# Kernel optimization log

Measured on AMD Instinct MI355X. Metric: run time of the kernel, lower is better.

The kernel has to match this reference:

```python
import jax, jax.numpy as jnp
import numpy as np

S = 4096
F = 512  # in_features, head_num == 1 so per-head dim == F


def setup_inputs() -> dict:
    key = jax.random.key(0)
    ks = jax.random.split(key, 11)
    std = 0.02
    inp = {
        "q": jax.random.normal(ks[0], (1, S, F), jnp.float32),
        "k": jax.random.normal(ks[1], (1, S, F), jnp.float32),
        "v": jax.random.normal(ks[2], (1, S, F), jnp.float32),
        "Wq": jax.random.normal(ks[3], (F, F), jnp.float32) * std,
        "bq": jax.random.normal(ks[4], (F,), jnp.float32) * std,
        "Wk": jax.random.normal(ks[5], (F, F), jnp.float32) * std,
        "bk": jax.random.normal(ks[6], (F,), jnp.float32) * std,
        "Wv": jax.random.normal(ks[7], (F, F), jnp.float32) * std,
        "bv": jax.random.normal(ks[8], (F,), jnp.float32) * std,
        "Wo": jax.random.normal(ks[9], (F, F), jnp.float32) * std,
        "bo": jax.random.normal(ks[10], (F,), jnp.float32) * std,
    }
    return inp


def reference(q, k, v, Wq, bq, Wk, bk, Wv, bv, Wo, bo):
    dk = Wq.shape[0]  # head_num == 1 -> per-head dim equals in_features
    # q_k, q_v: projections of q WITHOUT activation (as in original forward)
    q_k = q @ Wk.T + bk            # (1, S, F)
    q_v = q @ Wv.T + bv            # (1, S, F)
    # activated projections (F.relu)
    qq = jax.nn.relu(q @ Wq.T + bq)[0]  # (S, F)
    kk = jax.nn.relu(k @ Wk.T + bk)[0]  # (S, F)
    vv = jax.nn.relu(v @ Wv.T + bv)[0]  # (S, F)
    # diagonal of qq @ q_k^T, computed without materializing the SxS matrix
    q_att = jnp.sum(qq * q_k[0], axis=-1, keepdims=True)  # (S, 1)
    scores = jnp.einsum('sd,td->st', qq, kk)               # (S, S)
    scores = jnp.concatenate([scores, q_att], axis=-1)     # (S, S+1)
    scores = scores / np.sqrt(dk + 1).astype(np.float32)
    attn = jax.nn.softmax(scores, axis=-1)                 # (S, S+1)
    res = attn[:, :-1] @ vv                                # (S, F)
    res = q_v[0] * q_att + res                             # elementwise fusion
    y = res[None]                                          # (1, S, F)
    y = jax.nn.relu(y @ Wo.T + bo)
    return y
```

## Files before the change

### kernel.cpp

```cpp
#include <hip/hip_runtime.h>
#include <math.h>

#define S_LEN 4096
#define F_DIM 512
#define PSPLIT 8
#define FIXED_M 4.0f
#define SCALE_QK 0.04415108f

typedef __attribute__((ext_vector_type(8))) short bf16x8;
typedef __attribute__((ext_vector_type(4))) float f32x4;

__device__ __forceinline__ unsigned short f2bf(float x) {
    union { float f; unsigned u; } v; v.f = x;
    unsigned r = v.u + 0x7fffu + ((v.u >> 16) & 1u);
    return (unsigned short)(r >> 16);
}
__device__ __forceinline__ float bf2f(unsigned short b) {
    union { unsigned u; float f; } v; v.u = ((unsigned)b) << 16;
    return v.f;
}
__device__ __forceinline__ void load_lds16(const void* g, void* l) {
    __builtin_amdgcn_global_load_lds(
        (const __attribute__((address_space(1))) unsigned int*)g,
        (__attribute__((address_space(3))) unsigned int*)l, 16, 0, 0);
}

struct CastArgs {
    const float* src[7];
    unsigned short* dst[7];
    int n4[7];
};
__global__ void cast_all(CastArgs a) {
    int r = blockIdx.y;
    int i = blockIdx.x * blockDim.x + threadIdx.x;
    if (i >= a.n4[r]) return;
    float4 v = ((const float4*)a.src[r])[i];
    ushort4 o;
    o.x = f2bf(v.x); o.y = f2bf(v.y); o.z = f2bf(v.z); o.w = f2bf(v.w);
    ((ushort4*)a.dst[r])[i] = o;
}

__global__ void transpose_bf16(const unsigned short* __restrict__ src,
                               unsigned short* __restrict__ dst) {
    __shared__ __align__(16) unsigned short tile[64][72];
    const int s0 = blockIdx.x * 64, f0 = blockIdx.y * 64;
    const int tid = threadIdx.x;
#pragma unroll
    for (int it = 0; it < 2; ++it) {
        int u = it * 256 + tid;
        int r = u >> 3, c = (u & 7) * 8;
        *(uint4*)&tile[r][c] = *(const uint4*)(src + (size_t)(s0 + r) * F_DIM + f0 + c);
    }
    __syncthreads();
#pragma unroll
    for (int it = 0; it < 2; ++it) {
        int u = it * 256 + tid;
        int fl = u >> 3, sc = (u & 7) * 8;
        unsigned short tmp[8];
#pragma unroll
        for (int i = 0; i < 8; ++i) tmp[i] = tile[sc + i][fl];
        *(uint4*)(dst + (size_t)(f0 + fl) * S_LEN + s0 + sc) = *(uint4*)tmp;
    }
}

struct GemmDesc {
    const unsigned short* X;
    const unsigned short* W;
    const float* bias;
    unsigned short* out_bf;
    float* out_f32;
    int relu;
};
struct GemmArgs { GemmDesc d[5]; };

#define FRAGA(qm) { _Pragma("unroll") for (int mt = 0; mt < 4; ++mt) { \
    const int ro = (aw + (qm) * 64 + mt * 16) * 64 + rbase; \
    af[mt][0] = *(const bf16x8*)&Ac[ro + q0]; \
    af[mt][1] = *(const bf16x8*)&Ac[ro + q1]; } }

#define FRAGB(qn) { _Pragma("unroll") for (int nt = 0; nt < 2; ++nt) { \
    const int ro = (bw + (qn) * 32 + nt * 16) * 64 + rbase; \
    bf[nt][0] = *(const bf16x8*)&Bc[ro + q0]; \
    bf[nt][1] = *(const bf16x8*)&Bc[ro + q1]; } }

#define MMQ(qm, qn) { __builtin_amdgcn_s_setprio(1); \
    _Pragma("unroll") for (int kh = 0; kh < 2; ++kh) \
    _Pragma("unroll") for (int mt = 0; mt < 4; ++mt) \
    _Pragma("unroll") for (int nt = 0; nt < 2; ++nt) \
      acc[(qm) * 4 + mt][(qn) * 2 + nt] = __builtin_amdgcn_mfma_f32_16x16x32_bf16( \
          af[mt][kh], bf[nt][kh], acc[(qm) * 4 + mt][(qn) * 2 + nt], 0, 0, 0); \
    __builtin_amdgcn_s_setprio(0); }

__device__ __forceinline__ void kloop256(const unsigned short* __restrict__ A, int lda,
                                         const unsigned short* __restrict__ B, int ldb,
                                         int m0, int n0, int kbase,
                                         unsigned short* smem, f32x4 acc[8][4]) {
    const int tid = threadIdx.x;
    const int w = tid >> 6, l = tid & 63;
    const int ln = l & 15, quad = l >> 4, lnx = l & 7;
    const int wm = w >> 2, wn = w & 3;
    const int srow = l >> 3;
    const int scol = (lnx ^ srow) * 8;
    const int rbase = ln * 64;
    const int q0 = (quad ^ lnx) * 8;
    const int q1 = ((4 + quad) ^ lnx) * 8;
    unsigned short* As = smem;
    unsigned short* Bs = smem + 32768;
    const unsigned short* Asrc = A + (size_t)(m0 + srow) * lda + kbase + scol;
    const unsigned short* Bsrc = B + (size_t)(n0 + srow) * ldb + kbase + scol;

    auto stageA = [&](int dd, int ktn) {
#pragma unroll
        for (int j = 0; j < 4; ++j) {
            int chunk = w * 4 + j;
            load_lds16(Asrc + (size_t)(chunk * 8) * lda + ktn * 64,
                       &As[dd * 16384 + chunk * 512]);
        }
    };
    auto stageB = [&](int dd, int ktn) {
#pragma unroll
        for (int j = 0; j < 4; ++j) {
            int chunk = w * 4 + j;
            load_lds16(Bsrc + (size_t)(chunk * 8) * ldb + ktn * 64,
                       &Bs[dd * 16384 + chunk * 512]);
        }
    };

    stageA(0, 0); stageB(0, 0);
    asm volatile("s_waitcnt vmcnt(0)" ::: "memory");
    __builtin_amdgcn_s_barrier();

#pragma unroll
    for (int kt = 0; kt < 8; ++kt) {
        const int d = kt & 1;
        const unsigned short* Ac = &As[d * 16384];
        const unsigned short* Bc = &Bs[d * 16384];
        const int aw = wm * 128, bw = wn * 64;
        bf16x8 af[4][2], bf[2][2];

        FRAGA(0); FRAGB(0);
        if (kt < 7) { stageA(d ^ 1, kt + 1); stageB(d ^ 1, kt + 1); }
        __builtin_amdgcn_s_barrier();
        MMQ(0, 0);
        __builtin_amdgcn_s_barrier();

        FRAGB(1);
        __builtin_amdgcn_s_barrier();
        MMQ(0, 1);
        __builtin_amdgcn_s_barrier();

        FRAGA(1);
        __builtin_amdgcn_s_barrier();
        MMQ(1, 1);
        __builtin_amdgcn_s_barrier();

        FRAGB(0);
        __builtin_amdgcn_s_barrier();
        MMQ(1, 0);
        asm volatile("s_waitcnt vmcnt(0)" ::: "memory");
        __builtin_amdgcn_s_barrier();
    }
}

__launch_bounds__(512, 2)
__global__ void gemm_proj2(GemmArgs args) {
    extern __shared__ unsigned short smem[];
    const GemmDesc d = args.d[blockIdx.y >> 1];
    const int n0 = (blockIdx.y & 1) * 256;
    const int m0 = blockIdx.x * 256;
    f32x4 acc[8][4];
    f32x4 z = {0.f, 0.f, 0.f, 0.f};
#pragma unroll
    for (int i = 0; i < 8; ++i)
#pragma unroll
        for (int j = 0; j < 4; ++j) acc[i][j] = z;

    kloop256(d.X, F_DIM, d.W, F_DIM, m0, n0, 0, smem, acc);

    const int tid = threadIdx.x;
    const int w = tid >> 6, l = tid & 63, quad = l >> 4, ln = l & 15;
    const int wm = w >> 2, wn = w & 3;
#pragma unroll
    for (int mi = 0; mi < 8; ++mi)
#pragma unroll
        for (int ni = 0; ni < 4; ++ni)
#pragma unroll
            for (int r = 0; r < 4; ++r) {
                int row = m0 + wm * 128 + mi * 16 + quad * 4 + r;
                int col = n0 + wn * 64 + ni * 16 + ln;
                float vv = acc[mi][ni][r] + d.bias[col];
                if (d.relu) vv = fmaxf(vv, 0.f);
                if (d.out_bf)  d.out_bf[(size_t)row * F_DIM + col] = f2bf(vv);
                if (d.out_f32) d.out_f32[(size_t)row * F_DIM + col] = vv;
            }
}

__launch_bounds__(512, 2)
__global__ void gemm_exp2(const unsigned short* __restrict__ X,
                          const unsigned short* __restrict__ W,
                          unsigned short* __restrict__ P,
                          float* __restrict__ lpart) {
    extern __shared__ unsigned short smem[];
    const int m0 = blockIdx.x * 256, n0 = blockIdx.y * 256;
    f32x4 acc[8][4];
    f32x4 z = {0.f, 0.f, 0.f, 0.f};
#pragma unroll
    for (int i = 0; i < 8; ++i)
#pragma unroll
        for (int j = 0; j < 4; ++j) acc[i][j] = z;

    kloop256(X, F_DIM, W, F_DIM, m0, n0, 0, smem, acc);

    const int tid = threadIdx.x;
    const int w = tid >> 6, l = tid & 63, quad = l >> 4, ln = l & 15;
    const int wm = w >> 2, wn = w & 3;
#pragma unroll
    for (int mi = 0; mi < 8; ++mi)
#pragma unroll
        for (int r = 0; r < 4; ++r) {
            int row = m0 + wm * 128 + mi * 16 + quad * 4 + r;
            float rs = 0.f;
#pragma unroll
            for (int ni = 0; ni < 4; ++ni) {
                int col = n0 + wn * 64 + ni * 16 + ln;
                float p = __expf(acc[mi][ni][r] * SCALE_QK - FIXED_M);
                P[(size_t)row * S_LEN + col] = f2bf(p);
                rs += p;
            }
            rs += __shfl_xor(rs, 1);
            rs += __shfl_xor(rs, 2);
            rs += __shfl_xor(rs, 4);
            rs += __shfl_xor(rs, 8);
            if (ln == 0) lpart[(size_t)row * 64 + blockIdx.y * 4 + wn] = rs;
        }
}

__launch_bounds__(512, 2)
__global__ void gemm_pv2(const unsigned short* __restrict__ P,
                         const unsigned short* __restrict__ vt,
                         unsigned short* __restrict__ O_p) {
    extern __shared__ unsigned short smem[];
    const int nb = blockIdx.y & 1, split = blockIdx.y >> 1;
    const int m0 = blockIdx.x * 256, n0 = nb * 256;
    f32x4 acc[8][4];
    f32x4 z = {0.f, 0.f, 0.f, 0.f};
#pragma unroll
    for (int i = 0; i < 8; ++i)
#pragma unroll
        for (int j = 0; j < 4; ++j) acc[i][j] = z;

    kloop256(P, S_LEN, vt, S_LEN, m0, n0, split * (S_LEN / PSPLIT), smem, acc);

    unsigned short* Op = O_p + (size_t)split * S_LEN * F_DIM;
    const int tid = threadIdx.x;
    const int w = tid >> 6, l = tid & 63, quad = l >> 4, ln = l & 15;
    const int wm = w >> 2, wn = w & 3;
#pragma unroll
    for (int mi = 0; mi < 8; ++mi)
#pragma unroll
        for (int ni = 0; ni < 4; ++ni)
#pragma unroll
            for (int r = 0; r < 4; ++r) {
                int row = m0 + wm * 128 + mi * 16 + quad * 4 + r;
                int col = n0 + wn * 64 + ni * 16 + ln;
                Op[(size_t)row * F_DIM + col] = f2bf(acc[mi][ni][r]);
            }
}

#define GEMM_KLOOP(XPTR, LDX, WPTR, LDW, KBEG, KEND)                                  \
    for (int k0 = (KBEG); k0 < (KEND); k0 += 64) {                                    \
        __syncthreads();                                                              \
        _Pragma("unroll")                                                             \
        for (int i = 0; i < 2; ++i) {                                                 \
            int c = w * 2 + i;                                                        \
            _Pragma("unroll")                                                         \
            for (int kh = 0; kh < 2; ++kh) {                                          \
                load_lds16((XPTR) + (size_t)(m0 + c * 16 + ln) * (LDX) + k0 + kh * 32 + quad * 8, \
                           &As[(c * 2 + kh) * 512]);                                  \
                load_lds16((WPTR) + (size_t)(n0 + c * 16 + ln) * (LDW) + k0 + kh * 32 + quad * 8, \
                           &Bs[(c * 2 + kh) * 512]);                                  \
            }                                                                         \
        }                                                                             \
        __syncthreads();                                                              \
        _Pragma("unroll")                                                             \
        for (int kh = 0; kh < 2; ++kh) {                                              \
            bf16x8 af2[4], bfr2[4];                                                   \
            _Pragma("unroll")                                                         \
            for (int mt = 0; mt < 4; ++mt)                                            \
                af2[mt] = *(const bf16x8*)&As[((wr * 4 + mt) * 2 + kh) * 512 + l * 8]; \
            _Pragma("unroll")                                                         \
            for (int nt = 0; nt < 4; ++nt)                                            \
                bfr2[nt] = *(const bf16x8*)&Bs[((wc * 4 + nt) * 2 + kh) * 512 + l * 8]; \
            _Pragma("unroll")                                                         \
            for (int mt = 0; mt < 4; ++mt)                                            \
                _Pragma("unroll")                                                     \
                for (int nt = 0; nt < 4; ++nt)                                        \
                    acc[mt][nt] = __builtin_amdgcn_mfma_f32_16x16x32_bf16(            \
                        af2[mt], bfr2[nt], acc[mt][nt], 0, 0, 0);                     \
        }                                                                             \
    }

__launch_bounds__(256, 2)
__global__ void gemm_final(const unsigned short* __restrict__ X,
                           const unsigned short* __restrict__ W,
                           const float* __restrict__ bias,
                           float* __restrict__ out) {
    __shared__ __align__(16) unsigned short As[16 * 512];
    __shared__ __align__(16) unsigned short Bs[16 * 512];
    const int n0 = blockIdx.y * 128;
    const int m0 = blockIdx.x * 128;
    const int tid = threadIdx.x;
    const int w = tid >> 6, l = tid & 63, quad = l >> 4, ln = l & 15;
    const int wr = w >> 1, wc = w & 1;

    f32x4 acc[4][4];
    f32x4 zero4 = {0.f, 0.f, 0.f, 0.f};
#pragma unroll
    for (int i = 0; i < 4; ++i)
#pragma unroll
        for (int j = 0; j < 4; ++j) acc[i][j] = zero4;

    GEMM_KLOOP(X, F_DIM, W, F_DIM, 0, F_DIM)

#pragma unroll
    for (int mt = 0; mt < 4; ++mt)
#pragma unroll
        for (int nt = 0; nt < 4; ++nt)
#pragma unroll
            for (int r = 0; r < 4; ++r) {
                int row = m0 + wr * 64 + mt * 16 + quad * 4 + r;
                int col = n0 + wc * 64 + nt * 16 + ln;
                out[(size_t)row * F_DIM + col] =
                    fmaxf(acc[mt][nt][r] + bias[col], 0.f);
            }
}

__global__ void combine_kernel(const unsigned short* __restrict__ O_p,
                               const float* __restrict__ lpart,
                               const unsigned short* __restrict__ qq,
                               const unsigned short* __restrict__ qk,
                               const unsigned short* __restrict__ qv,
                               unsigned short* __restrict__ res_bf) {
    int row = blockIdx.x;
    int t = threadIdx.x;
    int wv = t >> 6, l = t & 63;
    __shared__ float ws[4];

    ushort4 a = *(const ushort4*)(qq + (size_t)row * F_DIM + t * 4);
    ushort4 b = *(const ushort4*)(qk + (size_t)row * F_DIM + t * 4);
    float dotp = bf2f(a.x) * bf2f(b.x) + bf2f(a.y) * bf2f(b.y) +
                 bf2f(a.z) * bf2f(b.z) + bf2f(a.w) * bf2f(b.w);
    float lp = (t < 64) ? lpart[(size_t)row * 64 + t] : 0.f;
#pragma unroll
    for (int off = 32; off >= 1; off >>= 1) {
        dotp += __shfl_xor(dotp, off);
        lp += __shfl_xor(lp, off);
    }
    if (l == 0) { ws[wv] = dotp; ws[2 + wv] = lp; }
    __syncthreads();
    float qa = ws[0] + ws[1];
    float denom = __expf(qa * SCALE_QK - FIXED_M) + ws[2] + ws[3];
    float inv = 1.f / denom;

    float4 s = {0.f, 0.f, 0.f, 0.f};
#pragma unroll
    for (int i = 0; i < PSPLIT; ++i) {
        ushort4 o = *(const ushort4*)(O_p + ((size_t)i * S_LEN + row) * F_DIM + t * 4);
        s.x += bf2f(o.x); s.y += bf2f(o.y); s.z += bf2f(o.z); s.w += bf2f(o.w);
    }
    ushort4 qvv = *(const ushort4*)(qv + (size_t)row * F_DIM + t * 4);
    ushort4 o;
    o.x = f2bf(bf2f(qvv.x) * qa + s.x * inv);
    o.y = f2bf(bf2f(qvv.y) * qa + s.y * inv);
    o.z = f2bf(bf2f(qvv.z) * qa + s.z * inv);
    o.w = f2bf(bf2f(qvv.w) * qa + s.w * inv);
    *(ushort4*)(res_bf + (size_t)row * F_DIM + t * 4) = o;
}

extern "C" void kernel_launch(void* const* d_in, const int* in_sizes, int n_in,
                              void* d_out, int out_size, void* d_ws, size_t ws_size,
                              hipStream_t stream) {
    const float* q  = (const float*)d_in[0];
    const float* k  = (const float*)d_in[1];
    const float* v  = (const float*)d_in[2];
    const float* Wq = (const float*)d_in[3];
    const float* bq = (const float*)d_in[4];
    const float* Wk = (const float*)d_in[5];
    const float* bk = (const float*)d_in[6];
    const float* Wv = (const float*)d_in[7];
    const float* bv = (const float*)d_in[8];
    const float* Wo = (const float*)d_in[9];
    const float* bo = (const float*)d_in[10];
    float* out = (float*)d_out;

    char* p = (char*)d_ws;
    auto alloc = [&](size_t bytes) -> char* {
        char* r = p; p += (bytes + 255) & ~(size_t)255; return r;
    };
    const size_t SF = (size_t)S_LEN * F_DIM;
    unsigned short* q_bf  = (unsigned short*)alloc(SF * 2);
    unsigned short* k_bf  = (unsigned short*)alloc(SF * 2);
    unsigned short* v_bf  = (unsigned short*)alloc(SF * 2);
    unsigned short* qq_bf = (unsigned short*)alloc(SF * 2);
    unsigned short* kk_bf = (unsigned short*)alloc(SF * 2);
    unsigned short* vv_bf = (unsigned short*)alloc(SF * 2);
    unsigned short* vt_bf = (unsigned short*)alloc(SF * 2);
    unsigned short* qk_bf = (unsigned short*)alloc(SF * 2);
    unsigned short* qv_bf = (unsigned short*)alloc(SF * 2);
    unsigned short* res_bf = (unsigned short*)alloc(SF * 2);
    unsigned short* wq_bf = (unsigned short*)alloc((size_t)F_DIM * F_DIM * 2);
    unsigned short* wk_bf = (unsigned short*)alloc((size_t)F_DIM * F_DIM * 2);
    unsigned short* wv_bf = (unsigned short*)alloc((size_t)F_DIM * F_DIM * 2);
    unsigned short* wo_bf = (unsigned short*)alloc((size_t)F_DIM * F_DIM * 2);
    unsigned short* P_bf  = (unsigned short*)alloc((size_t)S_LEN * S_LEN * 2);
    float* lpart = (float*)alloc((size_t)S_LEN * 64 * 4);
    unsigned short* O_p = (unsigned short*)alloc((size_t)PSPLIT * SF * 2);

    static int attr_done = 0;
    if (!attr_done) {
        hipFuncSetAttribute((const void*)gemm_proj2,
                            hipFuncAttributeMaxDynamicSharedMemorySize, 131072);
        hipFuncSetAttribute((const void*)gemm_exp2,
                            hipFuncAttributeMaxDynamicSharedMemorySize, 131072);
        hipFuncSetAttribute((const void*)gemm_pv2,
                            hipFuncAttributeMaxDynamicSharedMemorySize, 131072);
        attr_done = 1;
    }

    CastArgs ca;
    ca.src[0] = q;  ca.dst[0] = q_bf;  ca.n4[0] = (int)(SF / 4);
    ca.src[1] = k;  ca.dst[1] = k_bf;  ca.n4[1] = (int)(SF / 4);
    ca.src[2] = v;  ca.dst[2] = v_bf;  ca.n4[2] = (int)(SF / 4);
    ca.src[3] = Wq; ca.dst[3] = wq_bf; ca.n4[3] = F_DIM * F_DIM / 4;
    ca.src[4] = Wk; ca.dst[4] = wk_bf; ca.n4[4] = F_DIM * F_DIM / 4;
    ca.src[5] = Wv; ca.dst[5] = wv_bf; ca.n4[5] = F_DIM * F_DIM / 4;
    ca.src[6] = Wo; ca.dst[6] = wo_bf; ca.n4[6] = F_DIM * F_DIM / 4;
    cast_all<<<dim3((unsigned)(SF / 4 / 256), 7), 256, 0, stream>>>(ca);

    GemmArgs ga;
    ga.d[0] = { q_bf, wq_bf, bq, qq_bf, nullptr, 1 };
    ga.d[1] = { k_bf, wk_bf, bk, kk_bf, nullptr, 1 };
    ga.d[2] = { v_bf, wv_bf, bv, vv_bf, nullptr, 1 };
    ga.d[3] = { q_bf, wk_bf, bk, qk_bf, nullptr, 0 };
    ga.d[4] = { q_bf, wv_bf, bv, qv_bf, nullptr, 0 };
    gemm_proj2<<<dim3(S_LEN / 256, 10), 512, 131072, stream>>>(ga);

    transpose_bf16<<<dim3(S_LEN / 64, F_DIM / 64), 256, 0, stream>>>(vv_bf, vt_bf);

    gemm_exp2<<<dim3(S_LEN / 256, S_LEN / 256), 512, 131072, stream>>>(qq_bf, kk_bf, P_bf, lpart);

    gemm_pv2<<<dim3(S_LEN / 256, 2 * PSPLIT), 512, 131072, stream>>>(P_bf, vt_bf, O_p);

    combine_kernel<<<S_LEN, 128, 0, stream>>>(O_p, lpart, qq_bf, qk_bf, qv_bf, res_bf);

    gemm_final<<<dim3(S_LEN / 128, 4), 256, 0, stream>>>(res_bf, wo_bf, bo, out);
}
```

Baseline: 203.0 us.

## Interleave global-to-LDS prefetch loads across MMA phases with partial vmcnt waits

The 256x256 GEMM k-loop no longer issues all next-tile A/B loads at once and waits with vmcnt(0) at the end of each iteration. It now spreads the loads as pairs across the four MMA phases, reorders the chunks so each phase's fragments arrive first, and uses partial vmcnt waits. The goal is to overlap global-to-LDS traffic with compute and avoid a full memory drain every iteration. The risk is correctness if the chunk ordering or the wait counts do not match which data each fragment read needs.

```diff
diff --git a/kernel.cpp b/kernel.cpp
--- a/kernel.cpp
+++ b/kernel.cpp
@@ -109,24 +109,25 @@
     const unsigned short* Asrc = A + (size_t)(m0 + srow) * lda + kbase + scol;
     const unsigned short* Bsrc = B + (size_t)(n0 + srow) * ldb + kbase + scol;
 
-    auto stageA = [&](int dd, int ktn) {
-#pragma unroll
-        for (int j = 0; j < 4; ++j) {
-            int chunk = w * 4 + j;
-            load_lds16(Asrc + (size_t)(chunk * 8) * lda + ktn * 64,
-                       &As[dd * 16384 + chunk * 512]);
-        }
+    const int a0c0 = w, a0c1 = 16 + w;
+    const int a1c0 = 8 + w, a1c1 = 24 + w;
+    const int b0c0 = ((2 * w) & 3) + 8 * (w >> 1);
+    const int b0c1 = b0c0 + 1;
+    const int b1c0 = b0c0 + 4, b1c1 = b0c1 + 4;
+
+    auto stA = [&](int dd, int ktn, int c) {
+        load_lds16(Asrc + (size_t)(c * 8) * lda + ktn * 64,
+                   &As[dd * 16384 + c * 512]);
     };
-    auto stageB = [&](int dd, int ktn) {
-#pragma unroll
-        for (int j = 0; j < 4; ++j) {
-            int chunk = w * 4 + j;
-            load_lds16(Bsrc + (size_t)(chunk * 8) * ldb + ktn * 64,
-                       &Bs[dd * 16384 + chunk * 512]);
-        }
+    auto stB = [&](int dd, int ktn, int c) {
+        load_lds16(Bsrc + (size_t)(c * 8) * ldb + ktn * 64,
+                   &Bs[dd * 16384 + c * 512]);
     };
 
-    stageA(0, 0); stageB(0, 0);
+    stA(0, 0, a0c0); stA(0, 0, a0c1);
+    stB(0, 0, b0c0); stB(0, 0, b0c1);
+    stB(0, 0, b1c0); stB(0, 0, b1c1);
+    stA(0, 0, a1c0); stA(0, 0, a1c1);
     asm volatile("s_waitcnt vmcnt(0)" ::: "memory");
     __builtin_amdgcn_s_barrier();
 
@@ -138,26 +139,34 @@
         const int aw = wm * 128, bw = wn * 64;
         bf16x8 af[4][2], bf[2][2];
 
+        if (kt < 7) { stA(d ^ 1, kt + 1, a0c0); stA(d ^ 1, kt + 1, a0c1); }
+        if (kt >= 1 && kt < 7) { asm volatile("s_waitcnt vmcnt(6)" ::: "memory"); }
+        if (kt == 7)           { asm volatile("s_waitcnt vmcnt(4)" ::: "memory"); }
+        __builtin_amdgcn_s_barrier();
         FRAGA(0); FRAGB(0);
-        if (kt < 7) { stageA(d ^ 1, kt + 1); stageB(d ^ 1, kt + 1); }
-        __builtin_amdgcn_s_barrier();
         MMQ(0, 0);
         __builtin_amdgcn_s_barrier();
 
+        if (kt < 7) { stB(d ^ 1, kt + 1, b0c0); stB(d ^ 1, kt + 1, b0c1); }
+        if (kt >= 1 && kt < 7) { asm volatile("s_waitcnt vmcnt(6)" ::: "memory"); }
+        if (kt == 7)           { asm volatile("s_waitcnt vmcnt(2)" ::: "memory"); }
+        __builtin_amdgcn_s_barrier();
         FRAGB(1);
-        __builtin_amdgcn_s_barrier();
         MMQ(0, 1);
         __builtin_amdgcn_s_barrier();
 
+        if (kt < 7) { stB(d ^ 1, kt + 1, b1c0); stB(d ^ 1, kt + 1, b1c1); }
+        if (kt >= 1 && kt < 7) { asm volatile("s_waitcnt vmcnt(6)" ::: "memory"); }
+        if (kt == 7)           { asm volatile("s_waitcnt vmcnt(0)" ::: "memory"); }
+        __builtin_amdgcn_s_barrier();
         FRAGA(1);
-        __builtin_amdgcn_s_barrier();
         MMQ(1, 1);
         __builtin_amdgcn_s_barrier();
 
+        if (kt < 7) { stA(d ^ 1, kt + 1, a1c0); stA(d ^ 1, kt + 1, a1c1); }
+        __builtin_amdgcn_s_barrier();
         FRAGB(0);
-        __builtin_amdgcn_s_barrier();
         MMQ(1, 0);
-        asm volatile("s_waitcnt vmcnt(0)" ::: "memory");
         __builtin_amdgcn_s_barrier();
     }
 }
```

After: 198.9 us. -2.1%, faster.
